# Kernel optimization log

Hardware: AMD Instinct MI355X
Metric: run time of the kernel (lower is better)

The kernel has to match this reference:

```python
import jax, jax.numpy as jnp
import numpy as np

B, N, DIM, DD = 8, 4096, 512, 512
SCALE = DD ** -0.5


def setup_inputs() -> dict:
    key = jax.random.key(0)
    ks = jax.random.split(key, 8)
    x = jax.random.normal(ks[0], (B, N, DIM), dtype=jnp.float32)
    mask = jnp.ones((B, N), dtype=bool)
    # torch nn.Linear(dim, decode_dim, bias=False): weight [DD, DIM], y = x @ W.T
    Wq = jax.random.normal(ks[1], (DD, DIM), dtype=jnp.float32) * (DIM ** -0.5)
    Wk = jax.random.normal(ks[2], (DD, DIM), dtype=jnp.float32) * (DIM ** -0.5)
    Wv = jax.random.normal(ks[3], (DD, DIM), dtype=jnp.float32) * (DIM ** -0.5)
    Wr = jax.random.normal(ks[4], (DD, DD), dtype=jnp.float32) * (DD ** -0.5)
    w_alpha = jax.random.normal(ks[5], (DD,), dtype=jnp.float32)
    w_beta = jax.random.normal(ks[6], (DD,), dtype=jnp.float32)
    return {"x": x, "Wq": Wq, "Wk": Wk, "Wv": Wv, "Wr": Wr,
            "w_alpha": w_alpha, "w_beta": w_beta, "mask": mask}


def _masked_softmax_n(logits, mask):
    # softmax over axis=1 (N), with -inf where mask is False
    logits = jnp.where(mask[:, :, None], logits, -jnp.inf)
    return jax.nn.softmax(logits, axis=1)


def reference(x, Wq, Wk, Wv, Wr, w_alpha, w_beta, mask):
    q = jnp.einsum('bnf,df->bnd', x, Wq)          # [B,N,DD]
    k = jnp.einsum('bnf,df->bnd', x, Wk)
    v = jnp.einsum('bnf,df->bnd', x, Wv)
    alpha = _masked_softmax_n(q * w_alpha * SCALE, mask)   # [B,N,DD]
    global_query = jnp.einsum('bnd,bnd->bd', q, alpha)     # [B,DD]
    p = global_query[:, None, :] * k                       # [B,N,DD]
    beta = _masked_softmax_n(p * w_beta * SCALE, mask)
    global_key = jnp.einsum('bnd,bnd->bd', p, beta)        # [B,DD]
    kv = global_key[:, None, :] * v                        # [B,N,DD]
    out = jnp.einsum('bnd,ed->bne', kv, Wr) + q
    return out
```

## Files before the change

kernel.cpp:

```cpp
#include <hip/hip_runtime.h>

#define N_    4096
#define DD_   512
#define SCALE_ 0.044194173824159216f

typedef unsigned short u16;
typedef __attribute__((ext_vector_type(8))) short bf16x8;
typedef __attribute__((ext_vector_type(4))) float f32x4;

__device__ __forceinline__ float bf2f(u16 u) {
    union { unsigned i; float f; } c; c.i = ((unsigned)u) << 16; return c.f;
}
__device__ __forceinline__ u16 f2bf(float f) {
    union { float f; unsigned u; } c; c.f = f;
    unsigned r = c.u + 0x7FFFu + ((c.u >> 16) & 1u);
    return (u16)(r >> 16);
}
__device__ __forceinline__ void gl_lds(const u16* g, u16* l) {
    __builtin_amdgcn_global_load_lds(
        (const __attribute__((address_space(1))) void*)g,
        (__attribute__((address_space(3))) void*)l, 16, 0, 0);
}

__global__ void cvt_x(const float* __restrict__ s, u16* __restrict__ d)
{
    const size_t i = ((size_t)blockIdx.x * 256 + threadIdx.x) * 8;
    float4 f0 = *(const float4*)(s + i), f1 = *(const float4*)(s + i + 4);
    u16 o[8];
    o[0]=f2bf(f0.x); o[1]=f2bf(f0.y); o[2]=f2bf(f0.z); o[3]=f2bf(f0.w);
    o[4]=f2bf(f1.x); o[5]=f2bf(f1.y); o[6]=f2bf(f1.z); o[7]=f2bf(f1.w);
    *(uint4*)(d + i) = *(uint4*)o;
}

__global__ void cvt_w(const float* s0, const float* s1, u16* d0, u16* d1)
{
    const float* s = blockIdx.z ? s1 : s0;
    u16* d = blockIdx.z ? d1 : d0;
    const size_t i = ((size_t)blockIdx.x * 256 + threadIdx.x) * 8;
    float4 f0 = *(const float4*)(s + i), f1 = *(const float4*)(s + i + 4);
    u16 o[8];
    o[0]=f2bf(f0.x); o[1]=f2bf(f0.y); o[2]=f2bf(f0.z); o[3]=f2bf(f0.w);
    o[4]=f2bf(f1.x); o[5]=f2bf(f1.y); o[6]=f2bf(f1.z); o[7]=f2bf(f1.w);
    *(uint4*)(d + i) = *(uint4*)o;
}

__global__ __launch_bounds__(512, 2)
void gemm_red(const u16* __restrict__ A, const u16* __restrict__ Bt,
              const float* __restrict__ coefV, int mode,
              float* T1, float* T2)
{
    const int g = blockIdx.x;
    const int gs = (g & 7) * 32 + (g >> 3);
    const int tileM = gs >> 1;
    const int tileN = gs & 1;
    const int b = tileM >> 4;

    __shared__ __align__(16) char smem[65536];
    u16* As0 = (u16*)smem;
    u16* Bs0 = (u16*)(smem + 16384);
    u16* As1 = (u16*)(smem + 32768);
    u16* Bs1 = (u16*)(smem + 49152);
    float (*rs1)[256] = (float(*)[256])smem;
    float (*rs2)[256] = (float(*)[256])(smem + 8192);

    const int tid = threadIdx.x, wave = tid >> 6, lane = tid & 63;
    const int waveM = wave >> 2, waveN = wave & 3;
    const int l15 = lane & 15, quad = lane >> 4;
    const int l4r = lane >> 2, l4c = lane & 3;

    float cf[4];
    #pragma unroll
    for (int ni = 0; ni < 4; ++ni) {
        const int lcol = waveN * 64 + ni * 16 + l15;
        cf[ni] = mode ? coefV[b * 512 + tileN * 256 + lcol]
                      : coefV[tileN * 256 + lcol] * SCALE_;
    }

    const u16* aPtr = A  + (size_t)(tileM * 256 + wave * 32 + l4r) * 512 + l4c * 8;
    const u16* bPtr = Bt + (size_t)(tileN * 256 + wave * 32 + l4r) * 512 + l4c * 8;

    f32x4 acc[8][4] = {};

    auto STAGE = [&](int k0, u16* Asb, u16* Bsb) {
        gl_lds(aPtr + k0,        Asb + wave * 1024);
        gl_lds(aPtr + k0 + 8192, Asb + wave * 1024 + 512);
        gl_lds(bPtr + k0,        Bsb + wave * 1024);
        gl_lds(bPtr + k0 + 8192, Bsb + wave * 1024 + 512);
    };
    auto COMPUTE = [&](const u16* Ac, const u16* Bc) {
        bf16x8 af[8], bfr[4];
        #pragma unroll
        for (int mi = 0; mi < 8; ++mi)
            af[mi] = *(const bf16x8*)&Ac[(waveM * 128 + mi * 16 + l15) * 32 + quad * 8];
        #pragma unroll
        for (int ni = 0; ni < 4; ++ni)
            bfr[ni] = *(const bf16x8*)&Bc[(waveN * 64 + ni * 16 + l15) * 32 + quad * 8];
        #pragma unroll
        for (int mi = 0; mi < 8; ++mi)
            #pragma unroll
            for (int ni = 0; ni < 4; ++ni)
                acc[mi][ni] = __builtin_amdgcn_mfma_f32_16x16x32_bf16(
                    af[mi], bfr[ni], acc[mi][ni], 0, 0, 0);
    };

    STAGE(0, As0, Bs0);
    __syncthreads();
    for (int k0 = 0; k0 < 512; k0 += 64) {
        STAGE(k0 + 32, As1, Bs1);
        COMPUTE(As0, Bs0);
        __syncthreads();
        if (k0 + 64 < 512) STAGE(k0 + 64, As0, Bs0);
        COMPUTE(As1, Bs1);
        __syncthreads();
    }

    float s1[4] = {0.f, 0.f, 0.f, 0.f}, s2[4] = {0.f, 0.f, 0.f, 0.f};
    #pragma unroll
    for (int ni = 0; ni < 4; ++ni)
        #pragma unroll
        for (int mi = 0; mi < 8; ++mi)
            #pragma unroll
            for (int r = 0; r < 4; ++r) {
                float v = acc[mi][ni][r];
                float e = __expf(v * cf[ni]);
                s1[ni] += e; s2[ni] += v * e;
            }

    const int ridx = waveM * 4 + quad;
    #pragma unroll
    for (int ni = 0; ni < 4; ++ni) {
        const int lcol = waveN * 64 + ni * 16 + l15;
        rs1[ridx][lcol] = s1[ni]; rs2[ridx][lcol] = s2[ni];
    }
    __syncthreads();
    if (tid < 256) {
        float a1 = 0.f, a2 = 0.f;
        #pragma unroll
        for (int j = 0; j < 8; ++j) { a1 += rs1[j][tid]; a2 += rs2[j][tid]; }
        atomicAdd(&T1[b * 512 + tileN * 256 + tid], a1);
        atomicAdd(&T2[b * 512 + tileN * 256 + tid], a2);
    }
}

__global__ void comb1_k(const float* __restrict__ T1, const float* __restrict__ T2,
                        const float* __restrict__ wb, float* gq, float* coefK)
{
    const int i = blockIdx.x * 256 + threadIdx.x;
    const float g = T2[i] / T1[i];
    gq[i] = g;
    coefK[i] = g * wb[i & 511] * SCALE_;
}

__global__ void comb2_k(const float* __restrict__ T1, const float* __restrict__ T2,
                        const float* __restrict__ gq, float* gk)
{
    const int i = blockIdx.x * 256 + threadIdx.x;
    gk[i] = gq[i] * (T2[i] / T1[i]);
}

__global__ void transp_cvt(const float* __restrict__ Wv, u16* WvT)
{
    __shared__ float t[32][33];
    const int f0 = (blockIdx.x & 15) * 32, d0 = (blockIdx.x >> 4) * 32;
    const int c = threadIdx.x & 31, r0 = threadIdx.x >> 5;
    #pragma unroll
    for (int p = 0; p < 4; ++p)
        t[r0 + p * 8][c] = Wv[(size_t)(d0 + r0 + p * 8) * 512 + f0 + c];
    __syncthreads();
    #pragma unroll
    for (int p = 0; p < 4; ++p)
        WvT[(size_t)(f0 + r0 + p * 8) * 512 + d0 + c] = f2bf(t[c][r0 + p * 8]);
}

__global__ void scaleA(const float* __restrict__ Wr, const float* __restrict__ gk, u16* Ap)
{
    const size_t idx0 = ((size_t)blockIdx.x * 256 + threadIdx.x) * 8;
    const int b = (int)(idx0 >> 18);
    const int d = (int)(idx0 & 511);
    const size_t ed = idx0 & ((1u << 18) - 1);
    const float* g = gk + b * 512 + d;
    float4 a0 = *(const float4*)(Wr + ed), a1 = *(const float4*)(Wr + ed + 4);
    u16 o[8];
    o[0]=f2bf(a0.x*g[0]); o[1]=f2bf(a0.y*g[1]); o[2]=f2bf(a0.z*g[2]); o[3]=f2bf(a0.w*g[3]);
    o[4]=f2bf(a1.x*g[4]); o[5]=f2bf(a1.y*g[5]); o[6]=f2bf(a1.z*g[6]); o[7]=f2bf(a1.w*g[7]);
    *(uint4*)(Ap + idx0) = *(uint4*)o;
}

__global__ __launch_bounds__(256)
void gemm_w2(const u16* __restrict__ Ap, const u16* __restrict__ Bt,
             u16* __restrict__ C, const float* __restrict__ addF)
{
    const u16* A = Ap + (size_t)blockIdx.z * 262144;
    u16* Cb = C + (size_t)blockIdx.z * 262144;

    __shared__ __align__(16) char smem[32768];
    u16* As0 = (u16*)smem;
    u16* Bs0 = (u16*)(smem + 8192);
    u16* As1 = (u16*)(smem + 16384);
    u16* Bs1 = (u16*)(smem + 24576);

    const int tid = threadIdx.x, wave = tid >> 6, lane = tid & 63;
    const int waveM = wave >> 1, waveN = wave & 1;
    const int l15 = lane & 15, quad = lane >> 4;
    const int l4r = lane >> 2, l4c = lane & 3;
    const int tileN = blockIdx.x, tileM = blockIdx.y;

    f32x4 acc[4][4] = {};
    const u16* aPtr = A  + (size_t)(tileM * 128 + wave * 32 + l4r) * 512 + l4c * 8;
    const u16* bPtr = Bt + (size_t)(tileN * 128 + wave * 32 + l4r) * 512 + l4c * 8;

    auto STAGE = [&](int k0, u16* Asb, u16* Bsb) {
        gl_lds(aPtr + k0,        Asb + wave * 1024);
        gl_lds(aPtr + k0 + 8192, Asb + wave * 1024 + 512);
        gl_lds(bPtr + k0,        Bsb + wave * 1024);
        gl_lds(bPtr + k0 + 8192, Bsb + wave * 1024 + 512);
    };
    auto COMPUTE = [&](const u16* Ac, const u16* Bc) {
        bf16x8 af[4], bfr[4];
        #pragma unroll
        for (int mi = 0; mi < 4; ++mi)
            af[mi] = *(const bf16x8*)&Ac[(waveM * 64 + mi * 16 + l15) * 32 + quad * 8];
        #pragma unroll
        for (int ni = 0; ni < 4; ++ni)
            bfr[ni] = *(const bf16x8*)&Bc[(waveN * 64 + ni * 16 + l15) * 32 + quad * 8];
        #pragma unroll
        for (int mi = 0; mi < 4; ++mi)
            #pragma unroll
            for (int ni = 0; ni < 4; ++ni)
                acc[mi][ni] = __builtin_amdgcn_mfma_f32_16x16x32_bf16(
                    af[mi], bfr[ni], acc[mi][ni], 0, 0, 0);
    };

    STAGE(0, As0, Bs0);
    __syncthreads();
    for (int k0 = 0; k0 < 512; k0 += 64) {
        STAGE(k0 + 32, As1, Bs1);
        COMPUTE(As0, Bs0);
        __syncthreads();
        if (k0 + 64 < 512) STAGE(k0 + 64, As0, Bs0);
        COMPUTE(As1, Bs1);
        __syncthreads();
    }

    #pragma unroll
    for (int mi = 0; mi < 4; ++mi)
        #pragma unroll
        for (int ni = 0; ni < 4; ++ni) {
            const int row = tileM * 128 + waveM * 64 + mi * 16 + quad * 4;
            const int col = tileN * 128 + waveN * 64 + ni * 16 + l15;
            #pragma unroll
            for (int r = 0; r < 4; ++r) {
                float vv = acc[mi][ni][r] + addF[(size_t)(row + r) * 512 + col];
                Cb[(size_t)(row + r) * 512 + col] = f2bf(vv);
            }
        }
}

__global__ __launch_bounds__(512, 2)
void gemm_out(const u16* __restrict__ A, const u16* __restrict__ W2,
              float* __restrict__ out)
{
    const int g = blockIdx.x;
    const int gs = (g & 7) * 32 + (g >> 3);
    const int tileM = gs >> 1, tileN = gs & 1;
    const u16* Bt = W2 + (size_t)(tileM >> 4) * 262144;

    __shared__ __align__(16) char smem[65536];
    u16* As0 = (u16*)smem;
    u16* Bs0 = (u16*)(smem + 16384);
    u16* As1 = (u16*)(smem + 32768);
    u16* Bs1 = (u16*)(smem + 49152);
    float* eb = (float*)smem;

    const int tid = threadIdx.x, wave = tid >> 6, lane = tid & 63;
    const int waveM = wave >> 2, waveN = wave & 3;
    const int l15 = lane & 15, quad = lane >> 4;
    const int l4r = lane >> 2, l4c = lane & 3;

    const u16* aPtr = A  + (size_t)(tileM * 256 + wave * 32 + l4r) * 512 + l4c * 8;
    const u16* bPtr = Bt + (size_t)(tileN * 256 + wave * 32 + l4r) * 512 + l4c * 8;

    f32x4 acc[8][4] = {};

    auto STAGE = [&](int k0, u16* Asb, u16* Bsb) {
        gl_lds(aPtr + k0,        Asb + wave * 1024);
        gl_lds(aPtr + k0 + 8192, Asb + wave * 1024 + 512);
        gl_lds(bPtr + k0,        Bsb + wave * 1024);
        gl_lds(bPtr + k0 + 8192, Bsb + wave * 1024 + 512);
    };
    auto COMPUTE = [&](const u16* Ac, const u16* Bc) {
        bf16x8 af[8], bfr[4];
        #pragma unroll
        for (int mi = 0; mi < 8; ++mi)
            af[mi] = *(const bf16x8*)&Ac[(waveM * 128 + mi * 16 + l15) * 32 + quad * 8];
        #pragma unroll
        for (int ni = 0; ni < 4; ++ni)
            bfr[ni] = *(const bf16x8*)&Bc[(waveN * 64 + ni * 16 + l15) * 32 + quad * 8];
        #pragma unroll
        for (int mi = 0; mi < 8; ++mi)
            #pragma unroll
            for (int ni = 0; ni < 4; ++ni)
                acc[mi][ni] = __builtin_amdgcn_mfma_f32_16x16x32_bf16(
                    af[mi], bfr[ni], acc[mi][ni], 0, 0, 0);
    };

    STAGE(0, As0, Bs0);
    __syncthreads();
    for (int k0 = 0; k0 < 512; k0 += 64) {
        STAGE(k0 + 32, As1, Bs1);
        COMPUTE(As0, Bs0);
        __syncthreads();
        if (k0 + 64 < 512) STAGE(k0 + 64, As0, Bs0);
        COMPUTE(As1, Bs1);
        __syncthreads();
    }

    #pragma unroll
    for (int mi = 0; mi < 8; ++mi) {
        __syncthreads();
        #pragma unroll
        for (int ni = 0; ni < 4; ++ni) {
            const int srow = waveM * 16 + quad * 4;
            const int lcol = waveN * 64 + ni * 16 + l15;
            #pragma unroll
            for (int r = 0; r < 4; ++r)
                eb[(srow + r) * 260 + lcol] = acc[mi][ni][r];
        }
        __syncthreads();
        #pragma unroll
        for (int p = 0; p < 4; ++p) {
            const int lr = p * 8 + (tid >> 6);
            const int cp = (tid & 63) * 4;
            const int grow = tileM * 256 + (lr >> 4) * 128 + mi * 16 + (lr & 15);
            float4 vv = *(const float4*)&eb[lr * 260 + cp];
            *(float4*)&out[(size_t)grow * 512 + tileN * 256 + cp] = vv;
        }
    }
}

extern "C" void kernel_launch(void* const* d_in, const int* in_sizes, int n_in,
                              void* d_out, int out_size, void* d_ws, size_t ws_size,
                              hipStream_t stream)
{
    const float* x  = (const float*)d_in[0];
    const float* Wq = (const float*)d_in[1];
    const float* Wk = (const float*)d_in[2];
    const float* Wv = (const float*)d_in[3];
    const float* Wr = (const float*)d_in[4];
    const float* wa = (const float*)d_in[5];
    const float* wb = (const float*)d_in[6];
    float* out = (float*)d_out;

    char* ws = (char*)d_ws;
    float* TQ1   = (float*)(ws);
    float* TQ2   = (float*)(ws + 16 * 1024);
    float* TK1   = (float*)(ws + 32 * 1024);
    float* TK2   = (float*)(ws + 48 * 1024);
    float* gq    = (float*)(ws + 64 * 1024);
    float* coefK = (float*)(ws + 80 * 1024);
    float* gk    = (float*)(ws + 96 * 1024);
    u16*   WvT   = (u16*)  (ws + 112 * 1024);
    u16*   Wqb   = (u16*)  (ws + 624 * 1024);
    u16*   Wkb   = (u16*)  (ws + 1136 * 1024);
    u16*   Ap    = (u16*)  (ws + 1648 * 1024);
    u16*   W2    = (u16*)  (ws + 5744 * 1024);
    u16*   xb    = (u16*)  (ws + 9840 * 1024);

    hipMemsetAsync(TQ1, 0, 64 * 1024, stream);
    cvt_x<<<8192, 256, 0, stream>>>(x, xb);
    cvt_w<<<dim3(128, 1, 2), 256, 0, stream>>>(Wq, Wk, Wqb, Wkb);
    transp_cvt<<<256, 256, 0, stream>>>(Wv, WvT);

    gemm_red<<<256, 512, 0, stream>>>(xb, Wqb, wa, 0, TQ1, TQ2);
    comb1_k<<<16, 256, 0, stream>>>(TQ1, TQ2, wb, gq, coefK);
    gemm_red<<<256, 512, 0, stream>>>(xb, Wkb, coefK, 1, TK1, TK2);
    comb2_k<<<16, 256, 0, stream>>>(TK1, TK2, gq, gk);

    scaleA<<<1024, 256, 0, stream>>>(Wr, gk, Ap);
    gemm_w2<<<dim3(4, 4, 8), 256, 0, stream>>>(Ap, WvT, W2, Wq);

    gemm_out<<<256, 512, 0, stream>>>(xb, W2, out);
}
```

Measured before the change: 220.7 us.

## Switch gemm_red and gemm_out to triple-buffered LDS pipeline with vmcnt waits

Replaces the double-buffered K loop in two GEMM kernels with a three-stage ring buffer. Two stages are prefetched and partial s_waitcnt vmcnt(4) waits are used, so one stage of global-to-LDS loads stays in flight during compute. Shared memory grows from 64KB to 96KB per block, which may cut the 2-blocks-per-CU occupancy implied by launch_bounds. It also relies on vmcnt counting with direct-to-LDS loads being correct.

```diff
diff --git a/kernel.cpp b/kernel.cpp
--- a/kernel.cpp
+++ b/kernel.cpp
@@ -55,11 +55,7 @@
     const int tileN = gs & 1;
     const int b = tileM >> 4;
 
-    __shared__ __align__(16) char smem[65536];
-    u16* As0 = (u16*)smem;
-    u16* Bs0 = (u16*)(smem + 16384);
-    u16* As1 = (u16*)(smem + 32768);
-    u16* Bs1 = (u16*)(smem + 49152);
+    __shared__ __align__(16) char smem[98304];
     float (*rs1)[256] = (float(*)[256])smem;
     float (*rs2)[256] = (float(*)[256])(smem + 8192);
 
@@ -81,13 +77,17 @@
 
     f32x4 acc[8][4] = {};
 
-    auto STAGE = [&](int k0, u16* Asb, u16* Bsb) {
+    auto STAGE = [&](int k0, int bi) {
+        u16* Asb = (u16*)(smem + bi * 32768);
+        u16* Bsb = Asb + 8192;
         gl_lds(aPtr + k0,        Asb + wave * 1024);
         gl_lds(aPtr + k0 + 8192, Asb + wave * 1024 + 512);
         gl_lds(bPtr + k0,        Bsb + wave * 1024);
         gl_lds(bPtr + k0 + 8192, Bsb + wave * 1024 + 512);
     };
-    auto COMPUTE = [&](const u16* Ac, const u16* Bc) {
+    auto COMPUTE = [&](int bi) {
+        const u16* Ac = (const u16*)(smem + bi * 32768);
+        const u16* Bc = Ac + 8192;
         bf16x8 af[8], bfr[4];
         #pragma unroll
         for (int mi = 0; mi < 8; ++mi)
@@ -103,16 +103,26 @@
                     af[mi], bfr[ni], acc[mi][ni], 0, 0, 0);
     };
 
-    STAGE(0, As0, Bs0);
+    STAGE(0, 0);
+    STAGE(32, 1);
+    asm volatile("s_waitcnt vmcnt(4)" ::: "memory");
+    __builtin_amdgcn_s_barrier();
+
+    int bi = 0;
+    for (int t = 0; t < 14; ++t) {
+        int bs = bi + 2; if (bs >= 3) bs -= 3;
+        STAGE((t + 2) * 32, bs);
+        COMPUTE(bi);
+        asm volatile("s_waitcnt vmcnt(4)" ::: "memory");
+        __builtin_amdgcn_s_barrier();
+        ++bi; if (bi >= 3) bi = 0;
+    }
+    COMPUTE(bi);
+    asm volatile("s_waitcnt vmcnt(0)" ::: "memory");
+    __builtin_amdgcn_s_barrier();
+    ++bi; if (bi >= 3) bi = 0;
+    COMPUTE(bi);
     __syncthreads();
-    for (int k0 = 0; k0 < 512; k0 += 64) {
-        STAGE(k0 + 32, As1, Bs1);
-        COMPUTE(As0, Bs0);
-        __syncthreads();
-        if (k0 + 64 < 512) STAGE(k0 + 64, As0, Bs0);
-        COMPUTE(As1, Bs1);
-        __syncthreads();
-    }
 
     float s1[4] = {0.f, 0.f, 0.f, 0.f}, s2[4] = {0.f, 0.f, 0.f, 0.f};
     #pragma unroll
@@ -265,11 +275,7 @@
     const int tileM = gs >> 1, tileN = gs & 1;
     const u16* Bt = W2 + (size_t)(tileM >> 4) * 262144;
 
-    __shared__ __align__(16) char smem[65536];
-    u16* As0 = (u16*)smem;
-    u16* Bs0 = (u16*)(smem + 16384);
-    u16* As1 = (u16*)(smem + 32768);
-    u16* Bs1 = (u16*)(smem + 49152);
+    __shared__ __align__(16) char smem[98304];
     float* eb = (float*)smem;
 
     const int tid = threadIdx.x, wave = tid >> 6, lane = tid & 63;
@@ -282,13 +288,17 @@
 
     f32x4 acc[8][4] = {};
 
-    auto STAGE = [&](int k0, u16* Asb, u16* Bsb) {
+    auto STAGE = [&](int k0, int bi) {
+        u16* Asb = (u16*)(smem + bi * 32768);
+        u16* Bsb = Asb + 8192;
         gl_lds(aPtr + k0,        Asb + wave * 1024);
         gl_lds(aPtr + k0 + 8192, Asb + wave * 1024 + 512);
         gl_lds(bPtr + k0,        Bsb + wave * 1024);
         gl_lds(bPtr + k0 + 8192, Bsb + wave * 1024 + 512);
     };
-    auto COMPUTE = [&](const u16* Ac, const u16* Bc) {
+    auto COMPUTE = [&](int bi) {
+        const u16* Ac = (const u16*)(smem + bi * 32768);
+        const u16* Bc = Ac + 8192;
         bf16x8 af[8], bfr[4];
         #pragma unroll
         for (int mi = 0; mi < 8; ++mi)
@@ -304,16 +314,25 @@
                     af[mi], bfr[ni], acc[mi][ni], 0, 0, 0);
     };
 
-    STAGE(0, As0, Bs0);
-    __syncthreads();
-    for (int k0 = 0; k0 < 512; k0 += 64) {
-        STAGE(k0 + 32, As1, Bs1);
-        COMPUTE(As0, Bs0);
-        __syncthreads();
-        if (k0 + 64 < 512) STAGE(k0 + 64, As0, Bs0);
-        COMPUTE(As1, Bs1);
-        __syncthreads();
-    }
+    STAGE(0, 0);
+    STAGE(32, 1);
+    asm volatile("s_waitcnt vmcnt(4)" ::: "memory");
+    __builtin_amdgcn_s_barrier();
+
+    int bi = 0;
+    for (int t = 0; t < 14; ++t) {
+        int bs = bi + 2; if (bs >= 3) bs -= 3;
+        STAGE((t + 2) * 32, bs);
+        COMPUTE(bi);
+        asm volatile("s_waitcnt vmcnt(4)" ::: "memory");
+        __builtin_amdgcn_s_barrier();
+        ++bi; if (bi >= 3) bi = 0;
+    }
+    COMPUTE(bi);
+    asm volatile("s_waitcnt vmcnt(0)" ::: "memory");
+    __builtin_amdgcn_s_barrier();
+    ++bi; if (bi >= 3) bi = 0;
+    COMPUTE(bi);
 
     #pragma unroll
     for (int mi = 0; mi < 8; ++mi) {
```

After: 216.3 us. 2.0% less time.
